# Kernel tuning notes

Measured on AMD Instinct MI355X. Metric: run time of the kernel, lower is better.

The kernel has to match this reference:

```python
import jax, jax.numpy as jnp
import numpy as np

SEQ, DIN, DOUT, RANK = 8192, 4096, 4096, 16

def setup_inputs() -> dict:
    key = jax.random.key(0)
    ks = jax.random.split(key, 5)
    return {
        "x": jax.random.normal(ks[0], (SEQ, DIN), dtype=jnp.float32),
        "W": jax.random.normal(ks[1], (DIN, DOUT), dtype=jnp.float32) * (1.0 / np.sqrt(DIN)),
        "bias": jax.random.normal(ks[2], (DOUT,), dtype=jnp.float32),
        "A_buffer": jax.random.normal(ks[3], (DIN, RANK), dtype=jnp.float32) * (1.0 / np.sqrt(DIN)),
        "B_buffer": jax.random.normal(ks[4], (RANK, DOUT), dtype=jnp.float32),
    }

def reference(x, W, bias, A_buffer, B_buffer):
    # base linear GEMM: [seq, in] @ [in, out] -> [seq, out]
    base_output = jnp.dot(x, W)
    # LoRA path: two low-rank GEMMs fused-added onto base output
    lora_a = jnp.dot(x, A_buffer)            # [seq, rank]
    output = base_output + jnp.dot(lora_a, B_buffer)  # [seq, out]
    # module returns (output, output_bias) with bias passed through separately
    return (output, bias)
```

## Files before the change

### kernel.cpp

```cpp
#include <hip/hip_runtime.h>
#include <cstdint>
#include <cstddef>


#define SEQ  8192
#define DIN  4096
#define DOUT 4096
#define RANK 16

typedef __attribute__((ext_vector_type(8))) __bf16 bf16x8;
typedef __attribute__((ext_vector_type(4))) float f32x4;
typedef __attribute__((ext_vector_type(8))) unsigned short ushort8;

#define CAST_BLOCKS ((SEQ * DIN) / (256 * 8))
#define WEFF_BLOCKS ((DOUT / 64) * (DIN / 64))

__device__ __forceinline__ unsigned short f32_to_bf16_rne(float f) {
  union { float f; unsigned int u; } cv;
  cv.f = f;
  unsigned int u = cv.u;
  u += 0x7FFFu + ((u >> 16) & 1u);
  return (unsigned short)(u >> 16);
}

__global__ __launch_bounds__(256) void prep_kernel(
    const float* __restrict__ x, unsigned short* __restrict__ xb,
    const float* __restrict__ bias, float* __restrict__ bias_out,
    const float* __restrict__ W, const float* __restrict__ A,
    const float* __restrict__ B, unsigned short* __restrict__ WT) {
  __shared__ float sBf[RANK][64];
  __shared__ float sAf[64][RANK];
  __shared__ unsigned short sT[64][65];
  const int bid = blockIdx.x;
  const int t = threadIdx.x;

  if (bid < CAST_BLOCKS) {
    const int tid = bid * 256 + t;
    const float4* x4 = (const float4*)x;
    float4 v0 = x4[(size_t)tid * 2 + 0];
    float4 v1 = x4[(size_t)tid * 2 + 1];
    ushort8 o;
    o[0] = f32_to_bf16_rne(v0.x); o[1] = f32_to_bf16_rne(v0.y);
    o[2] = f32_to_bf16_rne(v0.z); o[3] = f32_to_bf16_rne(v0.w);
    o[4] = f32_to_bf16_rne(v1.x); o[5] = f32_to_bf16_rne(v1.y);
    o[6] = f32_to_bf16_rne(v1.z); o[7] = f32_to_bf16_rne(v1.w);
    *(ushort8*)(xb + (size_t)tid * 8) = o;
    if (tid < DOUT) bias_out[tid] = bias[tid];
    return;
  }

  const int b  = bid - CAST_BLOCKS;
  const int n0 = (b & 63) * 64;
  const int k0 = (b >> 6) * 64;

  for (int idx = t; idx < RANK * 64; idx += 256) {
    int r = idx >> 6, c = idx & 63;
    sBf[r][c] = B[(size_t)r * DOUT + n0 + c];
  }
  for (int idx = t; idx < 64 * RANK; idx += 256) {
    int i = idx >> 4, r = idx & 15;
    sAf[i][r] = A[(size_t)(k0 + i) * RANK + r];
  }
  __syncthreads();

  const int c   = t & 63;
  const int sub = t >> 6;
  #pragma unroll
  for (int p = 0; p < 16; ++p) {
    const int ki = p * 4 + sub;
    float acc = W[(size_t)(k0 + ki) * DOUT + n0 + c];
    #pragma unroll
    for (int r = 0; r < RANK; ++r) acc += sAf[ki][r] * sBf[r][c];
    sT[ki][c] = f32_to_bf16_rne(acc);
  }
  __syncthreads();
  #pragma unroll
  for (int p = 0; p < 16; ++p) {
    const int ni = p * 4 + sub;
    WT[(size_t)(n0 + ni) * DIN + k0 + c] = sT[c][ni];
  }
}

#define BM 128
#define BN 128
#define BK 64

__global__ __launch_bounds__(256) void gemm_bt_kernel(
    const unsigned short* __restrict__ xb, const unsigned short* __restrict__ wt,
    float* __restrict__ out) {
  __shared__ unsigned short sA[BM * BK];
  __shared__ unsigned short sB[BN * BK];
  const int t = threadIdx.x;
  const int n0 = blockIdx.x * BN;
  const int m0 = blockIdx.y * BM;

  const int lane = t & 63;
  const int w    = t >> 6;
  const int wr   = w >> 1;
  const int wc   = w & 1;
  const int quad = lane >> 4;
  const int lcol = lane & 15;

  const int g     = (lane & 7) ^ ((lane >> 3) & 7);
  const int rbase = w * 8 + (lane >> 3);
  const unsigned short* gA[4];
  const unsigned short* gB[4];
  #pragma unroll
  for (int j = 0; j < 4; ++j) {
    gA[j] = xb + (size_t)(m0 + rbase + j * 32) * DIN + g * 8;
    gB[j] = wt + (size_t)(n0 + rbase + j * 32) * DIN + g * 8;
  }
  unsigned short* lA[4];
  unsigned short* lB[4];
  #pragma unroll
  for (int j = 0; j < 4; ++j) {
    lA[j] = (unsigned short*)sA + (j * 256 + t) * 8;
    lB[j] = (unsigned short*)sB + (j * 256 + t) * 8;
  }

  f32x4 acc[4][4] = {};

  const int xorv = lcol & 7;
  const int arow = (wr * 64 + lcol) * BK;
  const int brow = (wc * 64 + lcol) * BK;

  for (int kt = 0; kt < DIN; kt += BK) {
    #pragma unroll
    for (int j = 0; j < 4; ++j)
      __builtin_amdgcn_global_load_lds(
          (const __attribute__((address_space(1))) void*)(gA[j] + kt),
          (__attribute__((address_space(3))) void*)lA[j], 16, 0, 0);
    #pragma unroll
    for (int j = 0; j < 4; ++j)
      __builtin_amdgcn_global_load_lds(
          (const __attribute__((address_space(1))) void*)(gB[j] + kt),
          (__attribute__((address_space(3))) void*)lB[j], 16, 0, 0);
    __syncthreads();

    #pragma unroll
    for (int kk = 0; kk < 2; ++kk) {
      const int cpos = ((quad + 4 * kk) ^ xorv) * 8;
      bf16x8 a[4], b[4];
      #pragma unroll
      for (int i = 0; i < 4; ++i)
        a[i] = *(const bf16x8*)((const unsigned short*)sA + arow + i * 16 * BK + cpos);
      #pragma unroll
      for (int j = 0; j < 4; ++j)
        b[j] = *(const bf16x8*)((const unsigned short*)sB + brow + j * 16 * BK + cpos);
      #pragma unroll
      for (int i = 0; i < 4; ++i)
        #pragma unroll
        for (int j = 0; j < 4; ++j)
          acc[i][j] = __builtin_amdgcn_mfma_f32_16x16x32_bf16(a[i], b[j], acc[i][j], 0, 0, 0);
    }
    __syncthreads();
  }

  const int row_base = m0 + wr * 64 + quad * 4;
  const int col_base = n0 + wc * 64 + lcol;
  #pragma unroll
  for (int i = 0; i < 4; ++i)
    #pragma unroll
    for (int j = 0; j < 4; ++j)
      #pragma unroll
      for (int r = 0; r < 4; ++r)
        out[(size_t)(row_base + i * 16 + r) * DOUT + (col_base + j * 16)] =
            acc[i][j][r];
}

extern "C" void kernel_launch(void* const* d_in, const int* in_sizes, int n_in,
                              void* d_out, int out_size, void* d_ws, size_t ws_size,
                              hipStream_t stream) {
  const float* x    = (const float*)d_in[0];
  const float* W    = (const float*)d_in[1];
  const float* bias = (const float*)d_in[2];
  const float* A    = (const float*)d_in[3];
  const float* B    = (const float*)d_in[4];
  float* out      = (float*)d_out;
  float* bias_out = out + (size_t)SEQ * DOUT;

  unsigned short* xb = (unsigned short*)d_ws;
  unsigned short* wt = xb + (size_t)SEQ * DIN;

  prep_kernel<<<CAST_BLOCKS + WEFF_BLOCKS, 256, 0, stream>>>(
      x, xb, bias, bias_out, W, A, B, wt);
  gemm_bt_kernel<<<dim3(DOUT / BN, SEQ / BM), 256, 0, stream>>>(xb, wt, out);
}
```

Before: 574.9 us.

## Rewrite bf16 GEMM as 256x256 double-buffered 8-wave pipeline with tile swizzle

The GEMM moves from 128x128 tiles with 4 waves and a single LDS buffer to 256x256 tiles with 8 waves and double-buffered LDS. The next K tile is loaded directly into LDS, interleaved with four MFMA phases per tile, using explicit vmcnt waits, raw barriers and s_setprio around MFMA bursts. A workgroup-ID swizzle is added for L2 locality. The aim is to hide global load latency and raise MFMA utilisation. The cost is heavy register use (128 accumulators per lane), 128KB of LDS per block, and fragile hand-tuned wait counts.

```diff
diff --git a/kernel.cpp b/kernel.cpp
--- a/kernel.cpp
+++ b/kernel.cpp
@@ -81,91 +81,143 @@
   }
 }
 
-#define BM 128
-#define BN 128
+#define BM 256
+#define BN 256
 #define BK 64
-
-__global__ __launch_bounds__(256) void gemm_bt_kernel(
+#define GRID_X (DOUT / BN)
+#define GRID_Y (SEQ / BM)
+#define NWG (GRID_X * GRID_Y)
+
+#define BARX()   asm volatile("s_barrier" ::: "memory")
+#define LGKM0()  asm volatile("s_waitcnt lgkmcnt(0)" ::: "memory")
+#define VM_CNT(n) asm volatile("s_waitcnt vmcnt(" #n ")" ::: "memory")
+
+#define STAGE_A(BUFSEL, Q, KOFF)                                              \
+  __builtin_amdgcn_global_load_lds(                                           \
+      (const __attribute__((address_space(1))) void*)(gA + (size_t)(Q) * 64 * DIN + (KOFF)), \
+      (__attribute__((address_space(3))) void*)(sA + (BUFSEL) * 16384 + (Q) * 4096 + t * 8), \
+      16, 0, 0);
+
+#define STAGE_B(BUFSEL, Q, KOFF)                                              \
+  __builtin_amdgcn_global_load_lds(                                           \
+      (const __attribute__((address_space(1))) void*)(gB + (size_t)(Q) * 64 * DIN + (KOFF)), \
+      (__attribute__((address_space(3))) void*)(sB + (BUFSEL) * 16384 + (Q) * 4096 + t * 8), \
+      16, 0, 0);
+
+#define STAGE_TILE(BUFSEL, KOFF)                                              \
+  STAGE_A(BUFSEL, 0, KOFF); STAGE_A(BUFSEL, 2, KOFF);                         \
+  STAGE_B(BUFSEL, 0, KOFF); STAGE_B(BUFSEL, 1, KOFF);                         \
+  STAGE_B(BUFSEL, 2, KOFF); STAGE_B(BUFSEL, 3, KOFF);                         \
+  STAGE_A(BUFSEL, 1, KOFF); STAGE_A(BUFSEL, 3, KOFF);
+
+#define MFMA16(BASE)                                                          \
+  _Pragma("unroll") for (int i_ = 0; i_ < 4; ++i_)                            \
+    _Pragma("unroll") for (int j_ = 0; j_ < 4; ++j_)                          \
+      acc[(BASE) + i_][j_] = __builtin_amdgcn_mfma_f32_16x16x32_bf16(         \
+          a[i_], b[j_], acc[(BASE) + i_][j_], 0, 0, 0);
+
+#define KTILE(ACUR, BCUR, DO_STAGE, NBUF, NKOFF, VMP1)                        \
+  {                                                                           \
+    bf16x8 a[4], b[4];                                                        \
+                                                 \
+    _Pragma("unroll") for (int i_ = 0; i_ < 4; ++i_)                          \
+      a[i_] = *(const bf16x8*)((ACUR) + aRow + i_ * 1024 + cpos0);            \
+    _Pragma("unroll") for (int j_ = 0; j_ < 4; ++j_)                          \
+      b[j_] = *(const bf16x8*)((BCUR) + bRow + j_ * 1024 + cpos0);            \
+    if (DO_STAGE) { STAGE_A(NBUF, 0, NKOFF); STAGE_A(NBUF, 2, NKOFF); }       \
+    VMP1;                                                                     \
+    BARX(); LGKM0();                                                          \
+    __builtin_amdgcn_s_setprio(1); MFMA16(0); __builtin_amdgcn_s_setprio(0);  \
+    BARX();                                                                   \
+                                                 \
+    _Pragma("unroll") for (int i_ = 0; i_ < 4; ++i_)                          \
+      a[i_] = *(const bf16x8*)((ACUR) + aRow + 4096 + i_ * 1024 + cpos0);     \
+    if (DO_STAGE) { STAGE_B(NBUF, 0, NKOFF); STAGE_B(NBUF, 1, NKOFF); }       \
+    BARX(); LGKM0();                                                          \
+    __builtin_amdgcn_s_setprio(1); MFMA16(4); __builtin_amdgcn_s_setprio(0);  \
+    BARX();                                                                   \
+                                                 \
+    _Pragma("unroll") for (int i_ = 0; i_ < 4; ++i_)                          \
+      a[i_] = *(const bf16x8*)((ACUR) + aRow + i_ * 1024 + cpos1);            \
+    _Pragma("unroll") for (int j_ = 0; j_ < 4; ++j_)                          \
+      b[j_] = *(const bf16x8*)((BCUR) + bRow + j_ * 1024 + cpos1);            \
+    if (DO_STAGE) { STAGE_B(NBUF, 2, NKOFF); STAGE_B(NBUF, 3, NKOFF); }       \
+    BARX(); LGKM0();                                                          \
+    __builtin_amdgcn_s_setprio(1); MFMA16(0); __builtin_amdgcn_s_setprio(0);  \
+    BARX();                                                                   \
+                                                 \
+    _Pragma("unroll") for (int i_ = 0; i_ < 4; ++i_)                          \
+      a[i_] = *(const bf16x8*)((ACUR) + aRow + 4096 + i_ * 1024 + cpos1);     \
+    if (DO_STAGE) { STAGE_A(NBUF, 1, NKOFF); STAGE_A(NBUF, 3, NKOFF); }       \
+    VM_CNT(2);                                                                \
+    BARX(); LGKM0();                                                          \
+    __builtin_amdgcn_s_setprio(1); MFMA16(4); __builtin_amdgcn_s_setprio(0);  \
+    BARX();                                                                   \
+  }
+
+__global__ __launch_bounds__(512, 2) void gemm_bt_kernel(
     const unsigned short* __restrict__ xb, const unsigned short* __restrict__ wt,
     float* __restrict__ out) {
-  __shared__ unsigned short sA[BM * BK];
-  __shared__ unsigned short sB[BN * BK];
+  __shared__ unsigned short sA[2 * BM * BK];
+  __shared__ unsigned short sB[2 * BN * BK];
+
   const int t = threadIdx.x;
-  const int n0 = blockIdx.x * BN;
-  const int m0 = blockIdx.y * BM;
-
   const int lane = t & 63;
   const int w    = t >> 6;
-  const int wr   = w >> 1;
-  const int wc   = w & 1;
+  const int wr   = w >> 2;
+  const int wc   = w & 3;
   const int quad = lane >> 4;
   const int lcol = lane & 15;
 
-  const int g     = (lane & 7) ^ ((lane >> 3) & 7);
-  const int rbase = w * 8 + (lane >> 3);
-  const unsigned short* gA[4];
-  const unsigned short* gB[4];
+  const int lid = blockIdx.y * GRID_X + blockIdx.x;
+  const int swz = (lid & 7) * (NWG / 8) + (lid >> 3);
+  const int n0 = (swz & (GRID_X - 1)) * BN;
+  const int m0 = (swz / GRID_X) * BM;
+
+  const int g    = (lane & 7) ^ (lane >> 3);
+  const int srow = w * 8 + (lane >> 3);
+  const unsigned short* gA = xb + (size_t)(m0 + srow) * DIN + g * 8;
+  const unsigned short* gB = wt + (size_t)(n0 + srow) * DIN + g * 8;
+
+  const int xorv  = lcol & 7;
+  const int cpos0 = (quad ^ xorv) * 8;
+  const int cpos1 = cpos0 ^ 32;
+  const int aRow  = (wr * 128 + lcol) * 64;
+  const int bRow  = (wc * 64  + lcol) * 64;
+
+  f32x4 acc[8][4] = {};
+
+  STAGE_TILE(0, 0);
+  STAGE_TILE(1, 64);
+  VM_CNT(8);
+  BARX();
+
+  KTILE(sA, sB, 0, 1, 64, ((void)0));
+
+  #pragma unroll 2
+  for (int tau = 1; tau < 63; ++tau) {
+    const unsigned short* Ac = sA + (tau & 1) * 16384;
+    const unsigned short* Bc = sB + (tau & 1) * 16384;
+    const int koff = (tau + 1) * 64;
+    KTILE(Ac, Bc, 1, ((tau + 1) & 1), koff, VM_CNT(2));
+  }
+
+  {
+    const unsigned short* Ac = sA + 16384;
+    const unsigned short* Bc = sB + 16384;
+    KTILE(Ac, Bc, 0, 0, 0, VM_CNT(0));
+  }
+
   #pragma unroll
-  for (int j = 0; j < 4; ++j) {
-    gA[j] = xb + (size_t)(m0 + rbase + j * 32) * DIN + g * 8;
-    gB[j] = wt + (size_t)(n0 + rbase + j * 32) * DIN + g * 8;
-  }
-  unsigned short* lA[4];
-  unsigned short* lB[4];
-  #pragma unroll
-  for (int j = 0; j < 4; ++j) {
-    lA[j] = (unsigned short*)sA + (j * 256 + t) * 8;
-    lB[j] = (unsigned short*)sB + (j * 256 + t) * 8;
-  }
-
-  f32x4 acc[4][4] = {};
-
-  const int xorv = lcol & 7;
-  const int arow = (wr * 64 + lcol) * BK;
-  const int brow = (wc * 64 + lcol) * BK;
-
-  for (int kt = 0; kt < DIN; kt += BK) {
-    #pragma unroll
-    for (int j = 0; j < 4; ++j)
-      __builtin_amdgcn_global_load_lds(
-          (const __attribute__((address_space(1))) void*)(gA[j] + kt),
-          (__attribute__((address_space(3))) void*)lA[j], 16, 0, 0);
-    #pragma unroll
-    for (int j = 0; j < 4; ++j)
-      __builtin_amdgcn_global_load_lds(
-          (const __attribute__((address_space(1))) void*)(gB[j] + kt),
-          (__attribute__((address_space(3))) void*)lB[j], 16, 0, 0);
-    __syncthreads();
-
-    #pragma unroll
-    for (int kk = 0; kk < 2; ++kk) {
-      const int cpos = ((quad + 4 * kk) ^ xorv) * 8;
-      bf16x8 a[4], b[4];
-      #pragma unroll
-      for (int i = 0; i < 4; ++i)
-        a[i] = *(const bf16x8*)((const unsigned short*)sA + arow + i * 16 * BK + cpos);
-      #pragma unroll
-      for (int j = 0; j < 4; ++j)
-        b[j] = *(const bf16x8*)((const unsigned short*)sB + brow + j * 16 * BK + cpos);
-      #pragma unroll
-      for (int i = 0; i < 4; ++i)
-        #pragma unroll
-        for (int j = 0; j < 4; ++j)
-          acc[i][j] = __builtin_amdgcn_mfma_f32_16x16x32_bf16(a[i], b[j], acc[i][j], 0, 0, 0);
-    }
-    __syncthreads();
-  }
-
-  const int row_base = m0 + wr * 64 + quad * 4;
-  const int col_base = n0 + wc * 64 + lcol;
-  #pragma unroll
-  for (int i = 0; i < 4; ++i)
+  for (int f = 0; f < 8; ++f) {
+    const int rb = m0 + wr * 128 + (f >> 2) * 64 + (f & 3) * 16 + quad * 4;
+    const int cb = n0 + wc * 64 + lcol;
     #pragma unroll
     for (int j = 0; j < 4; ++j)
       #pragma unroll
       for (int r = 0; r < 4; ++r)
-        out[(size_t)(row_base + i * 16 + r) * DOUT + (col_base + j * 16)] =
-            acc[i][j][r];
+        out[(size_t)(rb + r) * DOUT + cb + j * 16] = acc[f][j][r];
+  }
 }
 
 extern "C" void kernel_launch(void* const* d_in, const int* in_sizes, int n_in,
@@ -184,5 +236,5 @@
 
   prep_kernel<<<CAST_BLOCKS + WEFF_BLOCKS, 256, 0, stream>>>(
       x, xb, bias, bias_out, W, A, B, wt);
-  gemm_bt_kernel<<<dim3(DOUT / BN, SEQ / BM), 256, 0, stream>>>(xb, wt, out);
-}
+  gemm_bt_kernel<<<dim3(GRID_X, GRID_Y), 512, 0, stream>>>(xb, wt, out);
+}
```

Measured after the change: 551.0 us. 4.1% less time.
